# Kernel optimization log

Measured on AMD Instinct MI355X. Metric: run time of the kernel, lower is better.

## Reference

```python
import jax, jax.numpy as jnp
import numpy as np

N, E, F_IN, H, C = 50000, 800000, 64, 4, 32
NEG_SLOPE = 0.2  # PyG GATConv default negative_slope
LN_EPS = 1e-5


def setup_inputs() -> dict:
    key = jax.random.key(0)
    ks = jax.random.split(key, 8)
    s = 1.0 / np.sqrt(F_IN)
    return {
        "x": jax.random.normal(ks[0], (N, F_IN), jnp.float32),
        "edge_index": jax.random.randint(ks[1], (2, E), 0, N, jnp.int64),
        "W": jax.random.normal(ks[2], (F_IN, H * C), jnp.float32) * s,
        "att_src": jax.random.normal(ks[3], (H, C), jnp.float32) * s,
        "att_dst": jax.random.normal(ks[4], (H, C), jnp.float32) * s,
        "bias": jnp.zeros((H * C,), jnp.float32),
        "res_w": jax.random.normal(ks[5], (F_IN, H * C), jnp.float32) * s,
        "res_b": jnp.zeros((H * C,), jnp.float32),
        "ln_g": jnp.ones((H * C,), jnp.float32),
        "ln_b": jnp.zeros((H * C,), jnp.float32),
    }


def reference(x, edge_index, W, att_src, att_dst, bias, res_w, res_b, ln_g, ln_b):
    n = x.shape[0]
    # GATConv adds self-loops by default
    loop = jnp.arange(n, dtype=edge_index.dtype)
    src = jnp.concatenate([edge_index[0], loop])
    dst = jnp.concatenate([edge_index[1], loop])

    h = (x @ W).reshape(n, H, C)                      # [N,H,C]
    a_src = jnp.einsum('nhc,hc->nh', h, att_src)       # [N,H]
    a_dst = jnp.einsum('nhc,hc->nh', h, att_dst)

    e = a_src[src] + a_dst[dst]                        # [Etot,H]
    e = jnp.where(e >= 0, e, NEG_SLOPE * e)            # leaky_relu

    # segment softmax over destination nodes
    m = jax.ops.segment_max(e, dst, num_segments=n)    # [N,H]
    ex = jnp.exp(e - m[dst])
    denom = jax.ops.segment_sum(ex, dst, num_segments=n)
    alpha = ex / denom[dst]                            # [Etot,H]

    msg = h[src] * alpha[:, :, None]                   # [Etot,H,C]
    out = jax.ops.segment_sum(msg, dst, num_segments=n)  # [N,H,C]
    out = out.reshape(n, H * C) + bias

    # elu; dropout is identity in eval mode
    out = jnp.where(out > 0, out, jnp.expm1(out))
    out = out + (x @ res_w + res_b)                    # residual Linear

    mu = out.mean(-1, keepdims=True)
    var = ((out - mu) ** 2).mean(-1, keepdims=True)
    return ln_g * (out - mu) * jax.lax.rsqrt(var + LN_EPS) + ln_b
```

## Files before the change

kernel.cpp:

```cpp
#include <hip/hip_runtime.h>

#define F_IN 64
#define NH 4
#define HC 128
#define NEG_SLOPE 0.2f
#define LN_EPS 1e-5f
#define BUCKET 128
#define BKT_CAP 2560
#define NSC 128
#define KREG 28
#define KW_BLOCKS 64

typedef __bf16 bf16_8 __attribute__((ext_vector_type(8)));
typedef float  f32_4  __attribute__((ext_vector_type(4)));

__device__ inline int detect_is64(const int* __restrict__ ei, int E) {
    int lane = threadIdx.x & 63;
    long long stride = (2LL * E) / 65;
    int w = ei[(((long long)(lane + 1)) * stride) | 1];
    return __ballot(w != 0) == 0ULL;
}

__device__ inline unsigned bfpack(float a, float b) {
    unsigned ua = __float_as_uint(a), ub = __float_as_uint(b);
    ua = (ua + 0x7fffu + ((ua >> 16) & 1u)) >> 16;
    ub = (ub + 0x7fffu + ((ub >> 16) & 1u)) >> 16;
    return ua | (ub << 16);
}

__global__ __launch_bounds__(256) void k_prep(
    const float* __restrict__ W, const float* __restrict__ res_w,
    __bf16* __restrict__ wt, int* __restrict__ g_cnt)
{
    int idx = blockIdx.x * 256 + threadIdx.x;
    int ch = idx >> 6, k = idx & 63;
    const float* src = (ch < HC) ? W : res_w;
    wt[ch * 64 + k] = (__bf16)src[k * HC + (ch & (HC - 1))];
    if (idx < 512) g_cnt[idx] = 0;
}

__global__ __launch_bounds__(256) void k_main(
    const float* __restrict__ x, const __bf16* __restrict__ wt,
    const float* __restrict__ att_src, const float* __restrict__ att_dst,
    unsigned* __restrict__ h_bf, unsigned* __restrict__ r_bf,
    float* __restrict__ a_s, float* __restrict__ a_d, int n,
    const int* __restrict__ ei, int E,
    int* __restrict__ g_cnt, unsigned* __restrict__ epk, int chunk)
{
    __shared__ int bcur[512];
    __shared__ int adj[512];
    __shared__ int ss[256];

    if ((int)blockIdx.x >= NSC) {
        int tid = threadIdx.x;
        int wv_ = tid >> 6, lane = tid & 63;
        int col = lane & 15, quad = lane >> 4;
        int node = (blockIdx.x - NSC) * 64 + wv_ * 16 + col;
        int nrow = (node < n) ? node : (n - 1);

        bf16_8 bx0, bx1;
        {
            const float* xp = &x[nrow * F_IN + quad * 8];
            float4 p0 = *(const float4*)(xp);
            float4 p1 = *(const float4*)(xp + 4);
            float4 p2 = *(const float4*)(xp + 32);
            float4 p3 = *(const float4*)(xp + 36);
            bx0[0] = (__bf16)p0.x; bx0[1] = (__bf16)p0.y; bx0[2] = (__bf16)p0.z; bx0[3] = (__bf16)p0.w;
            bx0[4] = (__bf16)p1.x; bx0[5] = (__bf16)p1.y; bx0[6] = (__bf16)p1.z; bx0[7] = (__bf16)p1.w;
            bx1[0] = (__bf16)p2.x; bx1[1] = (__bf16)p2.y; bx1[2] = (__bf16)p2.z; bx1[3] = (__bf16)p2.w;
            bx1[4] = (__bf16)p3.x; bx1[5] = (__bf16)p3.y; bx1[6] = (__bf16)p3.z; bx1[7] = (__bf16)p3.w;
        }

        float vs[4] = {0.f, 0.f, 0.f, 0.f};
        float vd[4] = {0.f, 0.f, 0.f, 0.f};

#pragma unroll
        for (int mt = 0; mt < 16; ++mt) {
            const __bf16* ap = &wt[(mt * 16 + col) * 64 + quad * 8];
            bf16_8 a0 = *(const bf16_8*)ap;
            bf16_8 a1 = *(const bf16_8*)(ap + 32);
            f32_4 acc = {0.f, 0.f, 0.f, 0.f};
            acc = __builtin_amdgcn_mfma_f32_16x16x32_bf16(a0, bx0, acc, 0, 0, 0);
            acc = __builtin_amdgcn_mfma_f32_16x16x32_bf16(a1, bx1, acc, 0, 0, 0);
            int ch0 = mt * 16 + quad * 4;
            if (mt < 8) {
                float4 as4 = *(const float4*)&att_src[ch0];
                float4 ad4 = *(const float4*)&att_dst[ch0];
                int head = mt >> 1;
                vs[head] += acc[0] * as4.x + acc[1] * as4.y + acc[2] * as4.z + acc[3] * as4.w;
                vd[head] += acc[0] * ad4.x + acc[1] * ad4.y + acc[2] * ad4.z + acc[3] * ad4.w;
                if (node < n) {
                    uint2 pk = make_uint2(bfpack(acc[0], acc[1]), bfpack(acc[2], acc[3]));
                    *(uint2*)&h_bf[node * 64 + (ch0 >> 1)] = pk;
                }
            } else {
                if (node < n) {
                    uint2 pk = make_uint2(bfpack(acc[0], acc[1]), bfpack(acc[2], acc[3]));
                    *(uint2*)&r_bf[node * 64 + ((ch0 - 128) >> 1)] = pk;
                }
            }
        }

#pragma unroll
        for (int hh = 0; hh < NH; ++hh) {
            vs[hh] += __shfl_down(vs[hh], 32, 64);
            vs[hh] += __shfl_down(vs[hh], 16, 64);
            vd[hh] += __shfl_down(vd[hh], 32, 64);
            vd[hh] += __shfl_down(vd[hh], 16, 64);
        }
        if (quad == 0 && node < n) {
            *(float4*)&a_s[node * NH] = make_float4(vs[0], vs[1], vs[2], vs[3]);
            *(float4*)&a_d[node * NH] = make_float4(vd[0], vd[1], vd[2], vd[3]);
        }
        return;
    }

    int t = threadIdx.x;
    for (int i = t; i < 512; i += 256) bcur[i] = 0;
    __syncthreads();
    int is64 = detect_is64(ei, E);
    int base = blockIdx.x * chunk, end = min(E, base + chunk);

    unsigned rg[KREG];
#pragma unroll
    for (int i = 0; i < KREG; ++i) {
        int idx = base + i * 256 + t;
        unsigned ent = 0;
        if (idx < end) {
            int s = is64 ? ei[2 * idx] : ei[idx];
            int d = is64 ? ei[2 * (E + idx)] : ei[E + idx];
            ent = ((unsigned)d << 16) | (unsigned)s;
            atomicAdd(&bcur[d >> 7], 1);
        }
        rg[i] = ent;
    }
    __syncthreads();

    int b0 = 2 * t, b1 = 2 * t + 1;
    int f0 = bcur[b0], f1 = bcur[b1];
    ss[t] = f0 + f1;
    __syncthreads();
#pragma unroll
    for (int off = 1; off < 256; off <<= 1) {
        int u = (t >= off) ? ss[t - off] : 0;
        __syncthreads();
        ss[t] += u;
        __syncthreads();
    }
    int ebase = ss[t] - (f0 + f1);

    int g0 = (f0 > 0) ? atomicAdd(&g_cnt[b0], f0) : 0;
    int g1 = (f1 > 0) ? atomicAdd(&g_cnt[b1], f1) : 0;
    bcur[b0] = ebase;
    bcur[b1] = ebase + f0;
    adj[b0] = b0 * BKT_CAP + g0 - ebase;
    adj[b1] = b1 * BKT_CAP + g1 - (ebase + f0);
    __syncthreads();

#pragma unroll
    for (int i = 0; i < KREG; ++i) {
        int idx = base + i * 256 + t;
        if (idx < end) {
            unsigned ent = rg[i];
            int bb = ent >> 23;
            int p = atomicAdd(&bcur[bb], 1);
            int loc = adj[bb] + p;
            if (loc < (bb + 1) * BKT_CAP) epk[loc] = ent;
        }
    }
}

__global__ __launch_bounds__(256) void kd_sort(
    const int* __restrict__ g_cnt, const unsigned* __restrict__ epk,
    unsigned short* __restrict__ ssorted, unsigned* __restrict__ offdeg, int n)
{
    __shared__ int hist[BUCKET];
    __shared__ int sc[BUCKET];
    __shared__ int cur[BUCKET];
    int b = blockIdx.x, t = threadIdx.x;
    int m = g_cnt[b]; if (m > BKT_CAP) m = BKT_CAP;
    const unsigned* reg = epk + (size_t)b * BKT_CAP;
    if (t < BUCKET) hist[t] = 0;
    __syncthreads();
    for (int e = t; e < m; e += 256)
        atomicAdd(&hist[(reg[e] >> 16) & (BUCKET - 1)], 1);
    __syncthreads();
    if (t < BUCKET) sc[t] = (hist[t] + 1) & ~1;
    __syncthreads();
#pragma unroll
    for (int o = 1; o < BUCKET; o <<= 1) {
        int u = (t >= o && t < BUCKET) ? sc[t - o] : 0;
        __syncthreads();
        if (t < BUCKET) sc[t] += u;
        __syncthreads();
    }
    if (t < BUCKET) {
        int excl = sc[t] - ((hist[t] + 1) & ~1);
        cur[t] = excl;
        int d = b * BUCKET + t;
        if (d < n)
            offdeg[d] = ((unsigned)(b * BKT_CAP + excl) << 12) | (unsigned)hist[t];
    }
    __syncthreads();
    unsigned short* outp = ssorted + (size_t)b * BKT_CAP;
    for (int e = t; e < m; e += 256) {
        unsigned ent = reg[e];
        int p = atomicAdd(&cur[(ent >> 16) & (BUCKET - 1)], 1);
        outp[p] = (unsigned short)(ent & 0xffffu);
    }
}

__global__ __launch_bounds__(256) void k_agg(
    const unsigned* __restrict__ offdeg, const unsigned short* __restrict__ ssorted,
    const float* __restrict__ a_s, const float* __restrict__ a_d,
    const unsigned int* __restrict__ h_bf, const unsigned int* __restrict__ r_bf,
    const float* __restrict__ bias, const float* __restrict__ res_b,
    const float* __restrict__ ln_g, const float* __restrict__ ln_b,
    float* __restrict__ out, int n)
{
    int wv = threadIdx.x >> 6, lane = threadIdx.x & 63;
    int d = blockIdx.x * 4 + wv;
    if (d >= n) return;
    int eh = lane >> 4;
    int g  = lane & 15;
    int head = g >> 2;
    float ad = a_d[d * NH + head];

    float ac[8] = {0.f, 0.f, 0.f, 0.f, 0.f, 0.f, 0.f, 0.f};
    float denom = 0.f;

#define ACCUM(WW, VV)                                                      \
    do {                                                                   \
        ac[0] += (WW) * __uint_as_float((VV).x << 16);                     \
        ac[1] += (WW) * __uint_as_float((VV).x & 0xffff0000u);             \
        ac[2] += (WW) * __uint_as_float((VV).y << 16);                     \
        ac[3] += (WW) * __uint_as_float((VV).y & 0xffff0000u);             \
        ac[4] += (WW) * __uint_as_float((VV).z << 16);                     \
        ac[5] += (WW) * __uint_as_float((VV).z & 0xffff0000u);             \
        ac[6] += (WW) * __uint_as_float((VV).w << 16);                     \
        ac[7] += (WW) * __uint_as_float((VV).w & 0xffff0000u);             \
    } while (0)

    {
        float e = a_s[d * NH + head] + ad;
        e = fmaxf(e, NEG_SLOPE * e);
        float w = (eh == 0) ? __expf(e) : 0.f;
        uint4 hv = *(const uint4*)&h_bf[d * 64 + 4 * g];
        ACCUM(w, hv);
        denom += w;
    }

    unsigned od = offdeg[d];
    int deg = od & 4095;
    const unsigned short* sl = &ssorted[od >> 12];
    int k = 0;
    for (; k + 7 < deg; k += 8) {
        unsigned sp = *(const unsigned*)&sl[k + 2 * eh];
        int s0 = sp & 0xffffu, s1 = sp >> 16;
        float e0 = a_s[s0 * NH + head];
        float e1 = a_s[s1 * NH + head];
        uint4 v0 = *(const uint4*)&h_bf[s0 * 64 + 4 * g];
        uint4 v1 = *(const uint4*)&h_bf[s1 * 64 + 4 * g];
        e0 += ad; e0 = fmaxf(e0, NEG_SLOPE * e0);
        float w0 = __expf(e0);
        e1 += ad; e1 = fmaxf(e1, NEG_SLOPE * e1);
        float w1 = __expf(e1);
        denom += w0 + w1;
        ACCUM(w0, v0);
        ACCUM(w1, v1);
    }
    for (; k < deg; k += 4) {
        int idx = k + eh;
        int valid = idx < deg;
        int s0 = valid ? sl[idx] : 0;
        float e0 = a_s[s0 * NH + head] + ad;
        uint4 v0 = *(const uint4*)&h_bf[s0 * 64 + 4 * g];
        e0 = fmaxf(e0, NEG_SLOPE * e0);
        float w0 = valid ? __expf(e0) : 0.f;
        denom += w0;
        ACCUM(w0, v0);
    }
#undef ACCUM

#pragma unroll
    for (int j = 0; j < 8; ++j) {
        ac[j] += __shfl_xor(ac[j], 32, 64);
        ac[j] += __shfl_xor(ac[j], 16, 64);
    }
    denom += __shfl_xor(denom, 32, 64);
    denom += __shfl_xor(denom, 16, 64);

    int c0 = g * 8;
    float4 bi0 = *(const float4*)&bias[c0];
    float4 bi1 = *(const float4*)&bias[c0 + 4];
    float4 rb0 = *(const float4*)&res_b[c0];
    float4 rb1 = *(const float4*)&res_b[c0 + 4];
    uint4 rv = *(const uint4*)&r_bf[d * 64 + 4 * g];

    float inv = 1.f / denom;
    float o[8];
    o[0] = ac[0] * inv + bi0.x; o[1] = ac[1] * inv + bi0.y;
    o[2] = ac[2] * inv + bi0.z; o[3] = ac[3] * inv + bi0.w;
    o[4] = ac[4] * inv + bi1.x; o[5] = ac[5] * inv + bi1.y;
    o[6] = ac[6] * inv + bi1.z; o[7] = ac[7] * inv + bi1.w;
#pragma unroll
    for (int j = 0; j < 8; ++j)
        o[j] = (o[j] > 0.f) ? o[j] : (__expf(o[j]) - 1.f);
    o[0] += __uint_as_float(rv.x << 16) + rb0.x;
    o[1] += __uint_as_float(rv.x & 0xffff0000u) + rb0.y;
    o[2] += __uint_as_float(rv.y << 16) + rb0.z;
    o[3] += __uint_as_float(rv.y & 0xffff0000u) + rb0.w;
    o[4] += __uint_as_float(rv.z << 16) + rb1.x;
    o[5] += __uint_as_float(rv.z & 0xffff0000u) + rb1.y;
    o[6] += __uint_as_float(rv.w << 16) + rb1.z;
    o[7] += __uint_as_float(rv.w & 0xffff0000u) + rb1.w;

    float ps = o[0] + o[1] + o[2] + o[3] + o[4] + o[5] + o[6] + o[7];
#pragma unroll
    for (int off = 32; off > 0; off >>= 1) ps += __shfl_down(ps, off, 64);
    float mean = __shfl(ps, 0, 64) * (1.f / (4 * HC));
    float dv[8], pv = 0.f;
#pragma unroll
    for (int j = 0; j < 8; ++j) { dv[j] = o[j] - mean; pv += dv[j] * dv[j]; }
#pragma unroll
    for (int off = 32; off > 0; off >>= 1) pv += __shfl_down(pv, off, 64);
    float var = __shfl(pv, 0, 64) * (1.f / (4 * HC));
    float rs = rsqrtf(var + LN_EPS);
    if (eh == 0) {
        float4 gg0 = *(const float4*)&ln_g[c0];
        float4 gg1 = *(const float4*)&ln_g[c0 + 4];
        float4 lb0 = *(const float4*)&ln_b[c0];
        float4 lb1 = *(const float4*)&ln_b[c0 + 4];
        *(float4*)&out[d * HC + c0] =
            make_float4(gg0.x * dv[0] * rs + lb0.x, gg0.y * dv[1] * rs + lb0.y,
                        gg0.z * dv[2] * rs + lb0.z, gg0.w * dv[3] * rs + lb0.w);
        *(float4*)&out[d * HC + c0 + 4] =
            make_float4(gg1.x * dv[4] * rs + lb1.x, gg1.y * dv[5] * rs + lb1.y,
                        gg1.z * dv[6] * rs + lb1.z, gg1.w * dv[7] * rs + lb1.w);
    }
}

extern "C" void kernel_launch(void* const* d_in, const int* in_sizes, int n_in,
                              void* d_out, int out_size, void* d_ws, size_t ws_size,
                              hipStream_t stream) {
    const float* x       = (const float*)d_in[0];
    const int*   ei      = (const int*)d_in[1];
    const float* W       = (const float*)d_in[2];
    const float* att_src = (const float*)d_in[3];
    const float* att_dst = (const float*)d_in[4];
    const float* bias    = (const float*)d_in[5];
    const float* res_w   = (const float*)d_in[6];
    const float* res_b   = (const float*)d_in[7];
    const float* ln_g    = (const float*)d_in[8];
    const float* ln_b    = (const float*)d_in[9];
    float* out = (float*)d_out;

    int n = in_sizes[0] / F_IN;
    int E = in_sizes[1] / 2;
    int NB = (n + BUCKET - 1) / BUCKET;
    int chunk = (E + NSC - 1) / NSC;
    int nka = (n + 63) / 64;

    unsigned*       h_bf   = (unsigned*)d_ws;
    unsigned*       r_bf   = h_bf + (size_t)n * 64;
    float*          a_s    = (float*)(r_bf + (size_t)n * 64);
    float*          a_d    = a_s + (size_t)n * NH;
    int*            g_cnt  = (int*)(a_d + (size_t)n * NH);
    unsigned*       epk    = (unsigned*)(g_cnt + 512);
    unsigned short* ssd    = (unsigned short*)(epk + (size_t)NB * BKT_CAP);
    unsigned*       offdeg = (unsigned*)(ssd + (size_t)NB * BKT_CAP);
    __bf16*         wt     = (__bf16*)(offdeg + n);

    k_prep<<<KW_BLOCKS, 256, 0, stream>>>(W, res_w, wt, g_cnt);

    k_main<<<NSC + nka, 256, 0, stream>>>(
        x, wt, att_src, att_dst, h_bf, r_bf, a_s, a_d, n,
        ei, E, g_cnt, epk, chunk);

    kd_sort<<<NB, 256, 0, stream>>>(g_cnt, epk, ssd, offdeg, n);

    k_agg<<<(n + 3) / 4, 256, 0, stream>>>(offdeg, ssd, a_s, a_d, h_bf, r_bf,
                                           bias, res_b, ln_g, ln_b, out, n);
}
```

Baseline: 163.7 us.

## Fuse bucket sort into aggregation and drop global atomics and prep kernel

Edge bucketing now writes into fixed per-chunk slots (CCAP per chunk per bucket) with per-chunk counts, so no global atomic counter and no prefix scan across blocks are needed. The per-bucket counting sort now runs in LDS inside a new aggregation kernel, which then processes 64 destination nodes per block, 8 nodes per wave. The weight transpose/bf16 pack moves into the GEMM blocks of k_main, which removes the separate prep kernel and cuts the launch count from four to two. In exchange, each bucket's sort is done twice (once per half-block), each wave walks its nodes one after another, and chunks with more than CCAP edges in one bucket would drop edges.

```diff
diff --git a/kernel.cpp b/kernel.cpp
--- a/kernel.cpp
+++ b/kernel.cpp
@@ -6,10 +6,11 @@
 #define NEG_SLOPE 0.2f
 #define LN_EPS 1e-5f
 #define BUCKET 128
-#define BKT_CAP 2560
 #define NSC 128
-#define KREG 28
-#define KW_BLOCKS 64
+#define CCAP 40
+#define RSLOTS (NSC * CCAP)
+#define KREG 25
+#define SL_CAP 2816
 
 typedef __bf16 bf16_8 __attribute__((ext_vector_type(8)));
 typedef float  f32_4  __attribute__((ext_vector_type(4)));
@@ -28,31 +29,34 @@
     return ua | (ub << 16);
 }
 
-__global__ __launch_bounds__(256) void k_prep(
-    const float* __restrict__ W, const float* __restrict__ res_w,
-    __bf16* __restrict__ wt, int* __restrict__ g_cnt)
-{
-    int idx = blockIdx.x * 256 + threadIdx.x;
-    int ch = idx >> 6, k = idx & 63;
-    const float* src = (ch < HC) ? W : res_w;
-    wt[ch * 64 + k] = (__bf16)src[k * HC + (ch & (HC - 1))];
-    if (idx < 512) g_cnt[idx] = 0;
-}
-
 __global__ __launch_bounds__(256) void k_main(
-    const float* __restrict__ x, const __bf16* __restrict__ wt,
+    const float* __restrict__ x, const float* __restrict__ W,
+    const float* __restrict__ res_w,
     const float* __restrict__ att_src, const float* __restrict__ att_dst,
+    __bf16* __restrict__ wt,
     unsigned* __restrict__ h_bf, unsigned* __restrict__ r_bf,
     float* __restrict__ a_s, float* __restrict__ a_d, int n,
     const int* __restrict__ ei, int E,
-    int* __restrict__ g_cnt, unsigned* __restrict__ epk, int chunk)
+    int* __restrict__ counts, unsigned* __restrict__ epk, int chunk, int NB)
 {
     __shared__ int bcur[512];
-    __shared__ int adj[512];
-    __shared__ int ss[256];
 
     if ((int)blockIdx.x >= NSC) {
         int tid = threadIdx.x;
+#pragma unroll
+        for (int jj = 0; jj < 32; ++jj) {
+            int idx = jj * 256 + tid;
+            int ch = idx >> 5;
+            int j5 = idx & 31;
+            int k0 = j5 * 2;
+            const float* src = (ch < HC) ? W : res_w;
+            int cc = ch & (HC - 1);
+            float lo = src[k0 * HC + cc];
+            float hi = src[(k0 + 1) * HC + cc];
+            ((unsigned*)wt)[ch * 32 + j5] = bfpack(lo, hi);
+        }
+        __syncthreads();
+
         int wv_ = tid >> 6, lane = tid & 63;
         int col = lane & 15, quad = lane >> 4;
         int node = (blockIdx.x - NSC) * 64 + wv_ * 16 + col;
@@ -115,17 +119,17 @@
         return;
     }
 
-    int t = threadIdx.x;
-    for (int i = t; i < 512; i += 256) bcur[i] = 0;
+    int c = blockIdx.x, t = threadIdx.x;
+    for (int i = t; i < NB; i += 256) bcur[i] = 0;
     __syncthreads();
     int is64 = detect_is64(ei, E);
-    int base = blockIdx.x * chunk, end = min(E, base + chunk);
+    int base = c * chunk, end = min(E, base + chunk);
 
     unsigned rg[KREG];
 #pragma unroll
     for (int i = 0; i < KREG; ++i) {
         int idx = base + i * 256 + t;
-        unsigned ent = 0;
+        unsigned ent = 0xFFFFFFFFu;
         if (idx < end) {
             int s = is64 ? ei[2 * idx] : ei[idx];
             int d = is64 ? ei[2 * (E + idx)] : ei[E + idx];
@@ -136,55 +140,59 @@
     }
     __syncthreads();
 
-    int b0 = 2 * t, b1 = 2 * t + 1;
-    int f0 = bcur[b0], f1 = bcur[b1];
-    ss[t] = f0 + f1;
-    __syncthreads();
-#pragma unroll
-    for (int off = 1; off < 256; off <<= 1) {
-        int u = (t >= off) ? ss[t - off] : 0;
-        __syncthreads();
-        ss[t] += u;
-        __syncthreads();
-    }
-    int ebase = ss[t] - (f0 + f1);
-
-    int g0 = (f0 > 0) ? atomicAdd(&g_cnt[b0], f0) : 0;
-    int g1 = (f1 > 0) ? atomicAdd(&g_cnt[b1], f1) : 0;
-    bcur[b0] = ebase;
-    bcur[b1] = ebase + f0;
-    adj[b0] = b0 * BKT_CAP + g0 - ebase;
-    adj[b1] = b1 * BKT_CAP + g1 - (ebase + f0);
+    for (int bb = t; bb < NB; bb += 256) {
+        int f = bcur[bb]; if (f > CCAP) f = CCAP;
+        counts[c * NB + bb] = f;
+        bcur[bb] = 0;
+    }
     __syncthreads();
 
 #pragma unroll
     for (int i = 0; i < KREG; ++i) {
-        int idx = base + i * 256 + t;
-        if (idx < end) {
-            unsigned ent = rg[i];
+        unsigned ent = rg[i];
+        if (ent != 0xFFFFFFFFu) {
             int bb = ent >> 23;
             int p = atomicAdd(&bcur[bb], 1);
-            int loc = adj[bb] + p;
-            if (loc < (bb + 1) * BKT_CAP) epk[loc] = ent;
-        }
-    }
-}
-
-__global__ __launch_bounds__(256) void kd_sort(
-    const int* __restrict__ g_cnt, const unsigned* __restrict__ epk,
-    unsigned short* __restrict__ ssorted, unsigned* __restrict__ offdeg, int n)
+            if (p < CCAP)
+                epk[(size_t)bb * RSLOTS + c * CCAP + p] = ent & 0x007FFFFFu;
+        }
+    }
+}
+
+__global__ __launch_bounds__(512) void k_aggs(
+    const int* __restrict__ counts, const unsigned* __restrict__ epk,
+    const float* __restrict__ a_s, const float* __restrict__ a_d,
+    const unsigned int* __restrict__ h_bf, const unsigned int* __restrict__ r_bf,
+    const float* __restrict__ bias, const float* __restrict__ res_b,
+    const float* __restrict__ ln_g, const float* __restrict__ ln_b,
+    float* __restrict__ out, int n, int NB)
 {
-    __shared__ int hist[BUCKET];
-    __shared__ int sc[BUCKET];
-    __shared__ int cur[BUCKET];
-    int b = blockIdx.x, t = threadIdx.x;
-    int m = g_cnt[b]; if (m > BKT_CAP) m = BKT_CAP;
-    const unsigned* reg = epk + (size_t)b * BKT_CAP;
+    __shared__ unsigned short sl[SL_CAP];
+    __shared__ int cnt_s[NSC];
+    __shared__ int hist[BUCKET], sc[BUCKET], cur[BUCKET];
+    __shared__ unsigned offd[BUCKET];
+
+    int b = blockIdx.x >> 1, half = blockIdx.x & 1;
+    int t = threadIdx.x;
+    if (t < NSC) cnt_s[t] = counts[t * NB + b];
     if (t < BUCKET) hist[t] = 0;
     __syncthreads();
-    for (int e = t; e < m; e += 256)
-        atomicAdd(&hist[(reg[e] >> 16) & (BUCKET - 1)], 1);
-    __syncthreads();
+
+    unsigned rg[RSLOTS / 512];
+#pragma unroll
+    for (int i = 0; i < RSLOTS / 512; ++i) {
+        int slot = i * 512 + t;
+        int cdiv = slot / CCAP;
+        int j = slot - cdiv * CCAP;
+        unsigned ent = 0xFFFFFFFFu;
+        if (j < cnt_s[cdiv]) {
+            ent = epk[(size_t)b * RSLOTS + slot];
+            atomicAdd(&hist[ent >> 16], 1);
+        }
+        rg[i] = ent;
+    }
+    __syncthreads();
+
     if (t < BUCKET) sc[t] = (hist[t] + 1) & ~1;
     __syncthreads();
 #pragma unroll
@@ -197,37 +205,37 @@
     if (t < BUCKET) {
         int excl = sc[t] - ((hist[t] + 1) & ~1);
         cur[t] = excl;
-        int d = b * BUCKET + t;
-        if (d < n)
-            offdeg[d] = ((unsigned)(b * BKT_CAP + excl) << 12) | (unsigned)hist[t];
-    }
-    __syncthreads();
-    unsigned short* outp = ssorted + (size_t)b * BKT_CAP;
-    for (int e = t; e < m; e += 256) {
-        unsigned ent = reg[e];
-        int p = atomicAdd(&cur[(ent >> 16) & (BUCKET - 1)], 1);
-        outp[p] = (unsigned short)(ent & 0xffffu);
-    }
-}
-
-__global__ __launch_bounds__(256) void k_agg(
-    const unsigned* __restrict__ offdeg, const unsigned short* __restrict__ ssorted,
-    const float* __restrict__ a_s, const float* __restrict__ a_d,
-    const unsigned int* __restrict__ h_bf, const unsigned int* __restrict__ r_bf,
-    const float* __restrict__ bias, const float* __restrict__ res_b,
-    const float* __restrict__ ln_g, const float* __restrict__ ln_b,
-    float* __restrict__ out, int n)
-{
-    int wv = threadIdx.x >> 6, lane = threadIdx.x & 63;
-    int d = blockIdx.x * 4 + wv;
-    if (d >= n) return;
+        offd[t] = ((unsigned)excl << 16) | (unsigned)hist[t];
+    }
+    __syncthreads();
+
+#pragma unroll
+    for (int i = 0; i < RSLOTS / 512; ++i) {
+        unsigned ent = rg[i];
+        if (ent != 0xFFFFFFFFu) {
+            int p = atomicAdd(&cur[ent >> 16], 1);
+            if (p < SL_CAP) sl[p] = (unsigned short)(ent & 0xffffu);
+        }
+    }
+    __syncthreads();
+
+    int wvid = t >> 6, lane = t & 63;
     int eh = lane >> 4;
     int g  = lane & 15;
     int head = g >> 2;
-    float ad = a_d[d * NH + head];
-
-    float ac[8] = {0.f, 0.f, 0.f, 0.f, 0.f, 0.f, 0.f, 0.f};
-    float denom = 0.f;
+    int dbase = b * BUCKET + half * 64 + wvid * 8;
+
+    for (int jd = 0; jd < 8; ++jd) {
+        int d = dbase + jd;
+        if (d >= n) break;
+
+        unsigned od = offd[d & (BUCKET - 1)];
+        int deg = od & 0xffff;
+        int sbase = od >> 16;
+        float ad = a_d[d * NH + head];
+
+        float ac[8] = {0.f, 0.f, 0.f, 0.f, 0.f, 0.f, 0.f, 0.f};
+        float denom = 0.f;
 
 #define ACCUM(WW, VV)                                                      \
     do {                                                                   \
@@ -241,102 +249,100 @@
         ac[7] += (WW) * __uint_as_float((VV).w & 0xffff0000u);             \
     } while (0)
 
-    {
-        float e = a_s[d * NH + head] + ad;
-        e = fmaxf(e, NEG_SLOPE * e);
-        float w = (eh == 0) ? __expf(e) : 0.f;
-        uint4 hv = *(const uint4*)&h_bf[d * 64 + 4 * g];
-        ACCUM(w, hv);
-        denom += w;
-    }
-
-    unsigned od = offdeg[d];
-    int deg = od & 4095;
-    const unsigned short* sl = &ssorted[od >> 12];
-    int k = 0;
-    for (; k + 7 < deg; k += 8) {
-        unsigned sp = *(const unsigned*)&sl[k + 2 * eh];
-        int s0 = sp & 0xffffu, s1 = sp >> 16;
-        float e0 = a_s[s0 * NH + head];
-        float e1 = a_s[s1 * NH + head];
-        uint4 v0 = *(const uint4*)&h_bf[s0 * 64 + 4 * g];
-        uint4 v1 = *(const uint4*)&h_bf[s1 * 64 + 4 * g];
-        e0 += ad; e0 = fmaxf(e0, NEG_SLOPE * e0);
-        float w0 = __expf(e0);
-        e1 += ad; e1 = fmaxf(e1, NEG_SLOPE * e1);
-        float w1 = __expf(e1);
-        denom += w0 + w1;
-        ACCUM(w0, v0);
-        ACCUM(w1, v1);
-    }
-    for (; k < deg; k += 4) {
-        int idx = k + eh;
-        int valid = idx < deg;
-        int s0 = valid ? sl[idx] : 0;
-        float e0 = a_s[s0 * NH + head] + ad;
-        uint4 v0 = *(const uint4*)&h_bf[s0 * 64 + 4 * g];
-        e0 = fmaxf(e0, NEG_SLOPE * e0);
-        float w0 = valid ? __expf(e0) : 0.f;
-        denom += w0;
-        ACCUM(w0, v0);
-    }
+        {
+            float e = a_s[d * NH + head] + ad;
+            e = fmaxf(e, NEG_SLOPE * e);
+            float w = (eh == 0) ? __expf(e) : 0.f;
+            uint4 hv = *(const uint4*)&h_bf[d * 64 + 4 * g];
+            ACCUM(w, hv);
+            denom += w;
+        }
+
+        int k = 0;
+        for (; k + 7 < deg; k += 8) {
+            unsigned sp = *(const unsigned*)&sl[sbase + k + 2 * eh];
+            int s0 = sp & 0xffffu, s1 = sp >> 16;
+            float e0 = a_s[s0 * NH + head];
+            float e1 = a_s[s1 * NH + head];
+            uint4 v0 = *(const uint4*)&h_bf[s0 * 64 + 4 * g];
+            uint4 v1 = *(const uint4*)&h_bf[s1 * 64 + 4 * g];
+            e0 += ad; e0 = fmaxf(e0, NEG_SLOPE * e0);
+            float w0 = __expf(e0);
+            e1 += ad; e1 = fmaxf(e1, NEG_SLOPE * e1);
+            float w1 = __expf(e1);
+            denom += w0 + w1;
+            ACCUM(w0, v0);
+            ACCUM(w1, v1);
+        }
+        for (; k < deg; k += 4) {
+            int idx = k + eh;
+            int valid = idx < deg;
+            int s0 = valid ? sl[sbase + idx] : 0;
+            float e0 = a_s[s0 * NH + head] + ad;
+            uint4 v0 = *(const uint4*)&h_bf[s0 * 64 + 4 * g];
+            e0 = fmaxf(e0, NEG_SLOPE * e0);
+            float w0 = valid ? __expf(e0) : 0.f;
+            denom += w0;
+            ACCUM(w0, v0);
+        }
 #undef ACCUM
 
 #pragma unroll
-    for (int j = 0; j < 8; ++j) {
-        ac[j] += __shfl_xor(ac[j], 32, 64);
-        ac[j] += __shfl_xor(ac[j], 16, 64);
-    }
-    denom += __shfl_xor(denom, 32, 64);
-    denom += __shfl_xor(denom, 16, 64);
-
-    int c0 = g * 8;
-    float4 bi0 = *(const float4*)&bias[c0];
-    float4 bi1 = *(const float4*)&bias[c0 + 4];
-    float4 rb0 = *(const float4*)&res_b[c0];
-    float4 rb1 = *(const float4*)&res_b[c0 + 4];
-    uint4 rv = *(const uint4*)&r_bf[d * 64 + 4 * g];
-
-    float inv = 1.f / denom;
-    float o[8];
-    o[0] = ac[0] * inv + bi0.x; o[1] = ac[1] * inv + bi0.y;
-    o[2] = ac[2] * inv + bi0.z; o[3] = ac[3] * inv + bi0.w;
-    o[4] = ac[4] * inv + bi1.x; o[5] = ac[5] * inv + bi1.y;
-    o[6] = ac[6] * inv + bi1.z; o[7] = ac[7] * inv + bi1.w;
-#pragma unroll
-    for (int j = 0; j < 8; ++j)
-        o[j] = (o[j] > 0.f) ? o[j] : (__expf(o[j]) - 1.f);
-    o[0] += __uint_as_float(rv.x << 16) + rb0.x;
-    o[1] += __uint_as_float(rv.x & 0xffff0000u) + rb0.y;
-    o[2] += __uint_as_float(rv.y << 16) + rb0.z;
-    o[3] += __uint_as_float(rv.y & 0xffff0000u) + rb0.w;
-    o[4] += __uint_as_float(rv.z << 16) + rb1.x;
-    o[5] += __uint_as_float(rv.z & 0xffff0000u) + rb1.y;
-    o[6] += __uint_as_float(rv.w << 16) + rb1.z;
-    o[7] += __uint_as_float(rv.w & 0xffff0000u) + rb1.w;
-
-    float ps = o[0] + o[1] + o[2] + o[3] + o[4] + o[5] + o[6] + o[7];
-#pragma unroll
-    for (int off = 32; off > 0; off >>= 1) ps += __shfl_down(ps, off, 64);
-    float mean = __shfl(ps, 0, 64) * (1.f / (4 * HC));
-    float dv[8], pv = 0.f;
-#pragma unroll
-    for (int j = 0; j < 8; ++j) { dv[j] = o[j] - mean; pv += dv[j] * dv[j]; }
-#pragma unroll
-    for (int off = 32; off > 0; off >>= 1) pv += __shfl_down(pv, off, 64);
-    float var = __shfl(pv, 0, 64) * (1.f / (4 * HC));
-    float rs = rsqrtf(var + LN_EPS);
-    if (eh == 0) {
-        float4 gg0 = *(const float4*)&ln_g[c0];
-        float4 gg1 = *(const float4*)&ln_g[c0 + 4];
-        float4 lb0 = *(const float4*)&ln_b[c0];
-        float4 lb1 = *(const float4*)&ln_b[c0 + 4];
-        *(float4*)&out[d * HC + c0] =
-            make_float4(gg0.x * dv[0] * rs + lb0.x, gg0.y * dv[1] * rs + lb0.y,
-                        gg0.z * dv[2] * rs + lb0.z, gg0.w * dv[3] * rs + lb0.w);
-        *(float4*)&out[d * HC + c0 + 4] =
-            make_float4(gg1.x * dv[4] * rs + lb1.x, gg1.y * dv[5] * rs + lb1.y,
-                        gg1.z * dv[6] * rs + lb1.z, gg1.w * dv[7] * rs + lb1.w);
+        for (int j = 0; j < 8; ++j) {
+            ac[j] += __shfl_xor(ac[j], 32, 64);
+            ac[j] += __shfl_xor(ac[j], 16, 64);
+        }
+        denom += __shfl_xor(denom, 32, 64);
+        denom += __shfl_xor(denom, 16, 64);
+
+        int c0 = g * 8;
+        float4 bi0 = *(const float4*)&bias[c0];
+        float4 bi1 = *(const float4*)&bias[c0 + 4];
+        float4 rb0 = *(const float4*)&res_b[c0];
+        float4 rb1 = *(const float4*)&res_b[c0 + 4];
+        uint4 rv = *(const uint4*)&r_bf[d * 64 + 4 * g];
+
+        float inv = 1.f / denom;
+        float o[8];
+        o[0] = ac[0] * inv + bi0.x; o[1] = ac[1] * inv + bi0.y;
+        o[2] = ac[2] * inv + bi0.z; o[3] = ac[3] * inv + bi0.w;
+        o[4] = ac[4] * inv + bi1.x; o[5] = ac[5] * inv + bi1.y;
+        o[6] = ac[6] * inv + bi1.z; o[7] = ac[7] * inv + bi1.w;
+#pragma unroll
+        for (int j = 0; j < 8; ++j)
+            o[j] = (o[j] > 0.f) ? o[j] : (__expf(o[j]) - 1.f);
+        o[0] += __uint_as_float(rv.x << 16) + rb0.x;
+        o[1] += __uint_as_float(rv.x & 0xffff0000u) + rb0.y;
+        o[2] += __uint_as_float(rv.y << 16) + rb0.z;
+        o[3] += __uint_as_float(rv.y & 0xffff0000u) + rb0.w;
+        o[4] += __uint_as_float(rv.z << 16) + rb1.x;
+        o[5] += __uint_as_float(rv.z & 0xffff0000u) + rb1.y;
+        o[6] += __uint_as_float(rv.w << 16) + rb1.z;
+        o[7] += __uint_as_float(rv.w & 0xffff0000u) + rb1.w;
+
+        float ps = o[0] + o[1] + o[2] + o[3] + o[4] + o[5] + o[6] + o[7];
+#pragma unroll
+        for (int off = 32; off > 0; off >>= 1) ps += __shfl_down(ps, off, 64);
+        float mean = __shfl(ps, 0, 64) * (1.f / (4 * HC));
+        float dv[8], pv = 0.f;
+#pragma unroll
+        for (int j = 0; j < 8; ++j) { dv[j] = o[j] - mean; pv += dv[j] * dv[j]; }
+#pragma unroll
+        for (int off = 32; off > 0; off >>= 1) pv += __shfl_down(pv, off, 64);
+        float var = __shfl(pv, 0, 64) * (1.f / (4 * HC));
+        float rs = rsqrtf(var + LN_EPS);
+        if (eh == 0) {
+            float4 gg0 = *(const float4*)&ln_g[c0];
+            float4 gg1 = *(const float4*)&ln_g[c0 + 4];
+            float4 lb0 = *(const float4*)&ln_b[c0];
+            float4 lb1 = *(const float4*)&ln_b[c0 + 4];
+            *(float4*)&out[d * HC + c0] =
+                make_float4(gg0.x * dv[0] * rs + lb0.x, gg0.y * dv[1] * rs + lb0.y,
+                            gg0.z * dv[2] * rs + lb0.z, gg0.w * dv[3] * rs + lb0.w);
+            *(float4*)&out[d * HC + c0 + 4] =
+                make_float4(gg1.x * dv[4] * rs + lb1.x, gg1.y * dv[5] * rs + lb1.y,
+                            gg1.z * dv[6] * rs + lb1.z, gg1.w * dv[7] * rs + lb1.w);
+        }
     }
 }
 
@@ -361,24 +367,18 @@
     int chunk = (E + NSC - 1) / NSC;
     int nka = (n + 63) / 64;
 
-    unsigned*       h_bf   = (unsigned*)d_ws;
-    unsigned*       r_bf   = h_bf + (size_t)n * 64;
-    float*          a_s    = (float*)(r_bf + (size_t)n * 64);
-    float*          a_d    = a_s + (size_t)n * NH;
-    int*            g_cnt  = (int*)(a_d + (size_t)n * NH);
-    unsigned*       epk    = (unsigned*)(g_cnt + 512);
-    unsigned short* ssd    = (unsigned short*)(epk + (size_t)NB * BKT_CAP);
-    unsigned*       offdeg = (unsigned*)(ssd + (size_t)NB * BKT_CAP);
-    __bf16*         wt     = (__bf16*)(offdeg + n);
-
-    k_prep<<<KW_BLOCKS, 256, 0, stream>>>(W, res_w, wt, g_cnt);
+    unsigned*  h_bf   = (unsigned*)d_ws;
+    unsigned*  r_bf   = h_bf + (size_t)n * 64;
+    float*     a_s    = (float*)(r_bf + (size_t)n * 64);
+    float*     a_d    = a_s + (size_t)n * NH;
+    int*       counts = (int*)(a_d + (size_t)n * NH);
+    unsigned*  epk    = (unsigned*)(counts + NSC * NB);
+    __bf16*    wt     = (__bf16*)(epk + (size_t)NB * RSLOTS);
 
     k_main<<<NSC + nka, 256, 0, stream>>>(
-        x, wt, att_src, att_dst, h_bf, r_bf, a_s, a_d, n,
-        ei, E, g_cnt, epk, chunk);
-
-    kd_sort<<<NB, 256, 0, stream>>>(g_cnt, epk, ssd, offdeg, n);
-
-    k_agg<<<(n + 3) / 4, 256, 0, stream>>>(offdeg, ssd, a_s, a_d, h_bf, r_bf,
-                                           bias, res_b, ln_g, ln_b, out, n);
-}
+        x, W, res_w, att_src, att_dst, wt, h_bf, r_bf, a_s, a_d, n,
+        ei, E, counts, epk, chunk, NB);
+
+    k_aggs<<<2 * NB, 512, 0, stream>>>(counts, epk, a_s, a_d, h_bf, r_bf,
+                                       bias, res_b, ln_g, ln_b, out, n, NB);
+}
```

Measured after the change: 186.4 us. +13.9%, slower.
